# Kernel tuning notes

Hardware: AMD Instinct MI355X
Metric: run time of the kernel (lower is better)

The kernel has to match this reference:

```python
import jax, jax.numpy as jnp
import numpy as np

N_NODES = 100000
N_EDGES = 1600000
IN_F = 128
OUT_F = 128
EDGE_F = 16


def setup_inputs() -> dict:
    key = jax.random.key(0)
    ks = jax.random.split(key, 8)
    H = jax.random.normal(ks[0], (N_NODES, IN_F), dtype=jnp.float32)
    edge_index = jax.random.randint(ks[1], (2, N_EDGES), 0, N_ODES_ := N_NODES, dtype=jnp.int64) if False else jax.random.randint(ks[1], (2, N_EDGES), 0, N_NODES, dtype=jnp.int32).astype(jnp.int64)
    edge_attr = jax.random.normal(ks[2], (N_EDGES, EDGE_F), dtype=jnp.float32)
    We = jax.random.normal(ks[3], (EDGE_F, IN_F), dtype=jnp.float32) * (1.0 / np.sqrt(EDGE_F))
    be = jnp.zeros((IN_F,), dtype=jnp.float32)
    W1 = jax.random.normal(ks[4], (IN_F, OUT_F), dtype=jnp.float32) * (1.0 / np.sqrt(IN_F))
    b1 = jnp.zeros((OUT_F,), dtype=jnp.float32)
    W2 = jax.random.normal(ks[5], (OUT_F, OUT_F), dtype=jnp.float32) * (1.0 / np.sqrt(OUT_F))
    b2 = jnp.zeros((OUT_F,), dtype=jnp.float32)
    return {"H": H, "edge_index": edge_index, "edge_attr": edge_attr,
            "We": We, "be": be, "W1": W1, "b1": b1, "W2": W2, "b2": b2}


def reference(H, edge_index, edge_attr, We, be, W1, b1, W2, b2):
    # edge_mlp: Linear(edge_attr_dim -> in_features)
    edge_messages = edge_attr @ We + be                       # [E, in_f]
    # gather by src, add edge messages
    messages = H[edge_index[0]] + edge_messages               # [E, in_f]
    # scatter_add by dst with dim_size = N
    aggregated = jax.ops.segment_sum(messages, edge_index[1], num_segments=H.shape[0])  # [N, in_f]
    # node_mlp: Linear -> ReLU -> Linear
    h = jax.nn.relu(aggregated @ W1 + b1)                     # [N, out_f]
    out = h @ W2 + b2                                         # [N, out_f]
    return out
```

## Files before the change

### kernel.cpp

```cpp
#include <hip/hip_runtime.h>

#define IN_F 128
#define EF 16

typedef short bf16x8 __attribute__((ext_vector_type(8)));
typedef float f32x4  __attribute__((ext_vector_type(4)));

__device__ __forceinline__ unsigned short f2b(float f) {
    unsigned b = __float_as_uint(f);
    b += 0x7fffu + ((b >> 16) & 1u);
    return (unsigned short)(b >> 16);
}
__device__ __forceinline__ float blo(unsigned u) { return __uint_as_float(u << 16); }
__device__ __forceinline__ float bhi(unsigned u) { return __uint_as_float(u & 0xffff0000u); }


__global__ __launch_bounds__(256) void hist_kernel(
    const int* __restrict__ ei, int* __restrict__ counts, int E)
{
    int e = blockIdx.x * 256 + threadIdx.x;
    if (e >= E) return;
    atomicAdd(&counts[ei[E + e]], 1);
}

__global__ __launch_bounds__(256) void scan_blocks_kernel(
    const int* __restrict__ in, int* __restrict__ out,
    int* __restrict__ partials, int n)
{
    __shared__ int sdata[256];
    const int t = threadIdx.x;
    const int idx0 = blockIdx.x * 1024 + t * 4;
    int v[4];
    #pragma unroll
    for (int i = 0; i < 4; i++) { int idx = idx0 + i; v[i] = (idx < n) ? in[idx] : 0; }
    int s = v[0] + v[1] + v[2] + v[3];
    sdata[t] = s;
    __syncthreads();
    for (int off = 1; off < 256; off <<= 1) {
        int x = (t >= off) ? sdata[t - off] : 0;
        __syncthreads();
        sdata[t] += x;
        __syncthreads();
    }
    if (t == 255) partials[blockIdx.x] = sdata[255];
    int run = (t > 0) ? sdata[t - 1] : 0;
    #pragma unroll
    for (int i = 0; i < 4; i++) {
        int idx = idx0 + i;
        if (idx < n) out[idx] = run;
        run += v[i];
    }
}

__global__ void scan_partials_kernel(int* partials, int B)
{
    __shared__ int sdata[1024];
    const int t = threadIdx.x;
    sdata[t] = (t < B) ? partials[t] : 0;
    __syncthreads();
    for (int off = 1; off < 1024; off <<= 1) {
        int x = (t >= off) ? sdata[t - off] : 0;
        __syncthreads();
        sdata[t] += x;
        __syncthreads();
    }
    if (t < B) partials[t] = (t > 0) ? sdata[t - 1] : 0;
}

__global__ __launch_bounds__(256) void scan_add_kernel(
    int* __restrict__ out, const int* __restrict__ partials, int n)
{
    int idx = blockIdx.x * 256 + threadIdx.x;
    if (idx < n) out[idx] += partials[idx >> 10];
}

__global__ __launch_bounds__(256) void build_kernel(
    const int* __restrict__ ei, int2* __restrict__ sorted,
    const int* __restrict__ offsets, int* __restrict__ cursor, int E)
{
    int e = blockIdx.x * 256 + threadIdx.x;
    if (e >= E) return;
    int src = ei[e];
    int dst = ei[E + e];
    int pos = offsets[dst] + atomicAdd(&cursor[dst], 1);
    sorted[pos] = make_int2(src, e);
}

__global__ __launch_bounds__(256) void h2b_kernel(
    const float* __restrict__ H, unsigned short* __restrict__ Hb, int n4)
{
    int i = blockIdx.x * 256 + threadIdx.x;
    if (i >= n4) return;
    float4 v = ((const float4*)H)[i];
    ushort4 r;
    r.x = f2b(v.x); r.y = f2b(v.y); r.z = f2b(v.z); r.w = f2b(v.w);
    ((ushort4*)Hb)[i] = r;
}

__global__ __launch_bounds__(256) void gather_bf16_kernel(
    const unsigned short* __restrict__ Hb,
    const float* __restrict__ EA,
    const int2* __restrict__ sorted,
    const int* __restrict__ offsets,
    float* __restrict__ agg,
    float* __restrict__ aggE,
    float* __restrict__ degf,
    int N)
{
    int n = blockIdx.x * 4 + (threadIdx.x >> 6);
    if (n >= N) return;
    int lane = threadIdx.x & 63;
    int half = lane >> 5;
    int l32  = lane & 31;
    int s = offsets[n];
    int e_end = offsets[n + 1];
    float a0 = 0.f, a1 = 0.f, a2 = 0.f, a3 = 0.f, accE = 0.f;
    int i = s + half;
    for (; i + 6 < e_end; i += 8) {
        int2 s0 = sorted[i];
        int2 s1 = sorted[i + 2];
        int2 s2 = sorted[i + 4];
        int2 s3 = sorted[i + 6];
        uint2 u0 = *(const uint2*)(Hb + (long long)s0.x * IN_F + l32 * 4);
        uint2 u1 = *(const uint2*)(Hb + (long long)s1.x * IN_F + l32 * 4);
        uint2 u2 = *(const uint2*)(Hb + (long long)s2.x * IN_F + l32 * 4);
        uint2 u3 = *(const uint2*)(Hb + (long long)s3.x * IN_F + l32 * 4);
        float e0 = 0.f, e1 = 0.f, e2 = 0.f, e3 = 0.f;
        if (l32 < EF) {
            e0 = EA[(long long)s0.y * EF + l32];
            e1 = EA[(long long)s1.y * EF + l32];
            e2 = EA[(long long)s2.y * EF + l32];
            e3 = EA[(long long)s3.y * EF + l32];
        }
        a0 += (blo(u0.x) + blo(u1.x)) + (blo(u2.x) + blo(u3.x));
        a1 += (bhi(u0.x) + bhi(u1.x)) + (bhi(u2.x) + bhi(u3.x));
        a2 += (blo(u0.y) + blo(u1.y)) + (blo(u2.y) + blo(u3.y));
        a3 += (bhi(u0.y) + bhi(u1.y)) + (bhi(u2.y) + bhi(u3.y));
        accE += (e0 + e1) + (e2 + e3);
    }
    for (; i < e_end; i += 2) {
        int2 se = sorted[i];
        uint2 u = *(const uint2*)(Hb + (long long)se.x * IN_F + l32 * 4);
        a0 += blo(u.x); a1 += bhi(u.x); a2 += blo(u.y); a3 += bhi(u.y);
        if (l32 < EF) accE += EA[(long long)se.y * EF + l32];
    }
    a0 += __shfl_xor(a0, 32, 64);
    a1 += __shfl_xor(a1, 32, 64);
    a2 += __shfl_xor(a2, 32, 64);
    a3 += __shfl_xor(a3, 32, 64);
    accE += __shfl_xor(accE, 32, 64);
    if (half == 0) {
        *(float4*)(agg + (long long)n * IN_F + l32 * 4) = make_float4(a0, a1, a2, a3);
        if (l32 < EF) aggE[n * EF + l32] = accE;
        if (l32 == 0) degf[n] = (float)(e_end - s);
    }
}

__global__ __launch_bounds__(256) void gather_f32_kernel(
    const float* __restrict__ H,
    const float* __restrict__ EA,
    const int2* __restrict__ sorted,
    const int* __restrict__ offsets,
    float* __restrict__ agg,
    float* __restrict__ aggE,
    float* __restrict__ degf,
    int N)
{
    int n = blockIdx.x * 4 + (threadIdx.x >> 6);
    if (n >= N) return;
    int lane = threadIdx.x & 63;
    int half = lane >> 5;
    int l32  = lane & 31;
    int s = offsets[n];
    int e_end = offsets[n + 1];
    float4 acc = make_float4(0.f, 0.f, 0.f, 0.f);
    float accE = 0.f;
    int i = s + half;
    for (; i + 6 < e_end; i += 8) {
        int2 s0 = sorted[i];
        int2 s1 = sorted[i + 2];
        int2 s2 = sorted[i + 4];
        int2 s3 = sorted[i + 6];
        float4 v0 = *(const float4*)(H + (long long)s0.x * IN_F + l32 * 4);
        float4 v1 = *(const float4*)(H + (long long)s1.x * IN_F + l32 * 4);
        float4 v2 = *(const float4*)(H + (long long)s2.x * IN_F + l32 * 4);
        float4 v3 = *(const float4*)(H + (long long)s3.x * IN_F + l32 * 4);
        float e0 = 0.f, e1 = 0.f, e2 = 0.f, e3 = 0.f;
        if (l32 < EF) {
            e0 = EA[(long long)s0.y * EF + l32];
            e1 = EA[(long long)s1.y * EF + l32];
            e2 = EA[(long long)s2.y * EF + l32];
            e3 = EA[(long long)s3.y * EF + l32];
        }
        acc.x += (v0.x + v1.x) + (v2.x + v3.x);
        acc.y += (v0.y + v1.y) + (v2.y + v3.y);
        acc.z += (v0.z + v1.z) + (v2.z + v3.z);
        acc.w += (v0.w + v1.w) + (v2.w + v3.w);
        accE  += (e0 + e1) + (e2 + e3);
    }
    for (; i < e_end; i += 2) {
        int2 se = sorted[i];
        float4 v = *(const float4*)(H + (long long)se.x * IN_F + l32 * 4);
        acc.x += v.x; acc.y += v.y; acc.z += v.z; acc.w += v.w;
        if (l32 < EF) accE += EA[(long long)se.y * EF + l32];
    }
    acc.x += __shfl_xor(acc.x, 32, 64);
    acc.y += __shfl_xor(acc.y, 32, 64);
    acc.z += __shfl_xor(acc.z, 32, 64);
    acc.w += __shfl_xor(acc.w, 32, 64);
    accE  += __shfl_xor(accE, 32, 64);
    if (half == 0) {
        *(float4*)(agg + (long long)n * IN_F + l32 * 4) = acc;
        if (l32 < EF) aggE[n * EF + l32] = accE;
        if (l32 == 0) degf[n] = (float)(e_end - s);
    }
}

__global__ __launch_bounds__(256) void edge_scatter_kernel(
    const float* __restrict__ H,
    const int* __restrict__ ei,
    const float* __restrict__ EA,
    float* __restrict__ agg,
    float* __restrict__ aggE,
    float* __restrict__ deg,
    int E)
{
    long long gid = (long long)blockIdx.x * 256 + threadIdx.x;
    int e = (int)(gid >> 7);
    if (e >= E) return;
    int f = (int)(gid & 127);
    int src = ei[e];
    int dst = ei[E + e];
    float m = H[(long long)src * IN_F + f];
    atomicAdd(&agg[(long long)dst * IN_F + f], m);
    if (f < EF) atomicAdd(&aggE[dst * EF + f], EA[e * EF + f]);
    if (f == 0) atomicAdd(&deg[dst], 1.0f);
}


__global__ __launch_bounds__(256) void prep_kernel(
    const float* __restrict__ agg, const float* __restrict__ aggE,
    const float* __restrict__ degf,
    const float* __restrict__ We, const float* __restrict__ be,
    unsigned short* __restrict__ Ab, int N)
{
    int r = blockIdx.x * 8 + (threadIdx.x >> 5);
    if (r >= N) return;
    int c4 = (threadIdx.x & 31) * 4;
    float4 v = *(const float4*)&agg[(long long)r * IN_F + c4];
    float d = degf[r];
    float4 bev = *(const float4*)&be[c4];
    v.x += d * bev.x; v.y += d * bev.y; v.z += d * bev.z; v.w += d * bev.w;
    #pragma unroll
    for (int k = 0; k < EF; k++) {
        float a = aggE[r * EF + k];
        float4 w = *(const float4*)&We[k * IN_F + c4];
        v.x += a * w.x; v.y += a * w.y; v.z += a * w.z; v.w += a * w.w;
    }
    ushort4 o;
    o.x = f2b(v.x); o.y = f2b(v.y); o.z = f2b(v.z); o.w = f2b(v.w);
    *(ushort4*)&Ab[(long long)r * IN_F + c4] = o;
}

__global__ __launch_bounds__(256) void wt_cast_kernel(
    const float* __restrict__ W, unsigned short* __restrict__ Wt)
{
    int idx = blockIdx.x * 256 + threadIdx.x;
    int n = idx >> 7, k = idx & 127;
    Wt[n * IN_F + k] = f2b(W[k * IN_F + n]);
}

#define XPITCH 136
__global__ __launch_bounds__(256) void mlp_mfma_kernel(
    const unsigned short* __restrict__ Ab,
    const unsigned short* __restrict__ W1t,
    const unsigned short* __restrict__ W2t,
    const float* __restrict__ b1, const float* __restrict__ b2,
    float* __restrict__ out, int N)
{
    __shared__ unsigned short sW[128 * XPITCH];
    __shared__ unsigned short sX[64 * XPITCH];
    const int t    = threadIdx.x;
    const int tile = blockIdx.x * 64;
    const int lane = t & 63;
    const int wv   = t >> 6;
    const int quad = lane >> 4;
    const int lr   = lane & 15;
    const int M0   = wv * 16;

    {
        const uint4 z = make_uint4(0, 0, 0, 0);
        #pragma unroll
        for (int j = 0; j < 4; j++) {
            int idx = t + 256 * j;
            int row = idx >> 4, c = idx & 15;
            uint4 v = z;
            if (tile + row < N) v = ((const uint4*)Ab)[(long long)(tile + row) * 16 + c];
            ((uint4*)sX)[row * 17 + c] = v;
        }
        #pragma unroll
        for (int j = 0; j < 8; j++) {
            int idx = t + 256 * j;
            int row = idx >> 4, c = idx & 15;
            ((uint4*)sW)[row * 17 + c] = ((const uint4*)W1t)[idx];
        }
    }
    __syncthreads();

    f32x4 acc[8];
    bf16x8 af[4];
    const f32x4 zero = {0.f, 0.f, 0.f, 0.f};

    #pragma unroll
    for (int kt = 0; kt < 4; kt++)
        af[kt] = *(const bf16x8*)&sX[(M0 + lr) * XPITCH + kt * 32 + quad * 8];
    #pragma unroll
    for (int nt = 0; nt < 8; nt++) {
        acc[nt] = zero;
        #pragma unroll
        for (int kt = 0; kt < 4; kt++) {
            bf16x8 bf = *(const bf16x8*)&sW[(nt * 16 + lr) * XPITCH + kt * 32 + quad * 8];
            acc[nt] = __builtin_amdgcn_mfma_f32_16x16x32_bf16(af[kt], bf, acc[nt], 0, 0, 0);
        }
    }
    #pragma unroll
    for (int nt = 0; nt < 8; nt++) {
        int col = nt * 16 + lr;
        float bias = b1[col];
        #pragma unroll
        for (int r = 0; r < 4; r++) {
            float v = fmaxf(acc[nt][r] + bias, 0.f);
            sX[(M0 + quad * 4 + r) * XPITCH + col] = f2b(v);
        }
    }
    __syncthreads();
    #pragma unroll
    for (int j = 0; j < 8; j++) {
        int idx = t + 256 * j;
        int row = idx >> 4, c = idx & 15;
        ((uint4*)sW)[row * 17 + c] = ((const uint4*)W2t)[idx];
    }
    __syncthreads();

    #pragma unroll
    for (int kt = 0; kt < 4; kt++)
        af[kt] = *(const bf16x8*)&sX[(M0 + lr) * XPITCH + kt * 32 + quad * 8];
    #pragma unroll
    for (int nt = 0; nt < 8; nt++) {
        acc[nt] = zero;
        #pragma unroll
        for (int kt = 0; kt < 4; kt++) {
            bf16x8 bf = *(const bf16x8*)&sW[(nt * 16 + lr) * XPITCH + kt * 32 + quad * 8];
            acc[nt] = __builtin_amdgcn_mfma_f32_16x16x32_bf16(af[kt], bf, acc[nt], 0, 0, 0);
        }
    }
    #pragma unroll
    for (int nt = 0; nt < 8; nt++) {
        int col = nt * 16 + lr;
        float bias = b2[col];
        #pragma unroll
        for (int r = 0; r < 4; r++) {
            int row = tile + M0 + quad * 4 + r;
            if (row < N) out[(long long)row * IN_F + col] = acc[nt][r] + bias;
        }
    }
}

__global__ __launch_bounds__(256) void node_mlp_kernel(
    float* agg_out,
    const float* __restrict__ aggE,
    const float* __restrict__ degf,
    const float* __restrict__ We, const float* __restrict__ be,
    const float* __restrict__ W1, const float* __restrict__ b1,
    const float* __restrict__ W2, const float* __restrict__ b2,
    int N)
{
    __shared__ float sA[32][IN_F];
    __shared__ float sH[32][IN_F];
    const int t  = threadIdx.x;
    const int c4 = (t & 31) * 4;
    const int r0 = t >> 5;

    const int tile = blockIdx.x * 32;
    if (tile >= N) return;
    int rows = N - tile;
    if (rows > 32) rows = 32;

    {
        const float4 bev = *(const float4*)&be[c4];
        #pragma unroll
        for (int i = 0; i < 4; i++) {
            int rr = r0 + 8 * i;
            float4 v = make_float4(0.f, 0.f, 0.f, 0.f);
            if (rr < rows) {
                long long r = tile + rr;
                v = *(const float4*)&agg_out[r * IN_F + c4];
                float d = degf[r];
                v.x += d * bev.x; v.y += d * bev.y; v.z += d * bev.z; v.w += d * bev.w;
                #pragma unroll
                for (int k = 0; k < EF; k++) {
                    float a = aggE[r * EF + k];
                    float4 w = *(const float4*)&We[k * IN_F + c4];
                    v.x += a * w.x; v.y += a * w.y; v.z += a * w.z; v.w += a * w.w;
                }
            }
            *(float4*)&sA[rr][c4] = v;
        }
    }
    __syncthreads();
    {
        const float4 bv = *(const float4*)&b1[c4];
        float4 a0 = bv, a1 = bv, a2 = bv, a3 = bv;
        for (int k = 0; k < IN_F; k++) {
            float4 w = *(const float4*)&W1[k * IN_F + c4];
            float x0 = sA[r0][k], x1 = sA[r0 + 8][k], x2 = sA[r0 + 16][k], x3 = sA[r0 + 24][k];
            a0.x += x0 * w.x; a0.y += x0 * w.y; a0.z += x0 * w.z; a0.w += x0 * w.w;
            a1.x += x1 * w.x; a1.y += x1 * w.y; a1.z += x1 * w.z; a1.w += x1 * w.w;
            a2.x += x2 * w.x; a2.y += x2 * w.y; a2.z += x2 * w.z; a2.w += x2 * w.w;
            a3.x += x3 * w.x; a3.y += x3 * w.y; a3.z += x3 * w.z; a3.w += x3 * w.w;
        }
        a0.x = fmaxf(a0.x, 0.f); a0.y = fmaxf(a0.y, 0.f); a0.z = fmaxf(a0.z, 0.f); a0.w = fmaxf(a0.w, 0.f);
        a1.x = fmaxf(a1.x, 0.f); a1.y = fmaxf(a1.y, 0.f); a1.z = fmaxf(a1.z, 0.f); a1.w = fmaxf(a1.w, 0.f);
        a2.x = fmaxf(a2.x, 0.f); a2.y = fmaxf(a2.y, 0.f); a2.z = fmaxf(a2.z, 0.f); a2.w = fmaxf(a2.w, 0.f);
        a3.x = fmaxf(a3.x, 0.f); a3.y = fmaxf(a3.y, 0.f); a3.z = fmaxf(a3.z, 0.f); a3.w = fmaxf(a3.w, 0.f);
        *(float4*)&sH[r0][c4]      = a0;
        *(float4*)&sH[r0 + 8][c4]  = a1;
        *(float4*)&sH[r0 + 16][c4] = a2;
        *(float4*)&sH[r0 + 24][c4] = a3;
    }
    __syncthreads();
    {
        const float4 bv = *(const float4*)&b2[c4];
        float4 a0 = bv, a1 = bv, a2 = bv, a3 = bv;
        for (int k = 0; k < IN_F; k++) {
            float4 w = *(const float4*)&W2[k * IN_F + c4];
            float x0 = sH[r0][k], x1 = sH[r0 + 8][k], x2 = sH[r0 + 16][k], x3 = sH[r0 + 24][k];
            a0.x += x0 * w.x; a0.y += x0 * w.y; a0.z += x0 * w.z; a0.w += x0 * w.w;
            a1.x += x1 * w.x; a1.y += x1 * w.y; a1.z += x1 * w.z; a1.w += x1 * w.w;
            a2.x += x2 * w.x; a2.y += x2 * w.y; a2.z += x2 * w.z; a2.w += x2 * w.w;
            a3.x += x3 * w.x; a3.y += x3 * w.y; a3.z += x3 * w.z; a3.w += x3 * w.w;
        }
        #pragma unroll
        for (int i = 0; i < 4; i++) {
            int rr = r0 + 8 * i;
            if (rr < rows) {
                float4 v = (i == 0) ? a0 : (i == 1) ? a1 : (i == 2) ? a2 : a3;
                *(float4*)&agg_out[(long long)(tile + rr) * IN_F + c4] = v;
            }
        }
    }
}

extern "C" void kernel_launch(void* const* d_in, const int* in_sizes, int n_in,
                              void* d_out, int out_size, void* d_ws, size_t ws_size,
                              hipStream_t stream) {
    const float* H  = (const float*)d_in[0];
    const int*   ei = (const int*)d_in[1];
    const float* EA = (const float*)d_in[2];
    const float* We = (const float*)d_in[3];
    const float* be = (const float*)d_in[4];
    const float* W1 = (const float*)d_in[5];
    const float* b1 = (const float*)d_in[6];
    const float* W2 = (const float*)d_in[7];
    const float* b2 = (const float*)d_in[8];
    float* out = (float*)d_out;

    const int N = in_sizes[0] / IN_F;
    const int E = in_sizes[2] / EF;

    char* p = (char*)d_ws;
    auto alloc = [&](size_t bytes) { char* r = p; p += (bytes + 255) & ~(size_t)255; return r; };
    int2*  sorted   = (int2*)alloc((size_t)E * sizeof(int2));
    float* aggE     = (float*)alloc((size_t)N * EF * sizeof(float));
    float* degf     = (float*)alloc((size_t)N * sizeof(float));
    int*   counts   = (int*)alloc((size_t)(N + 1) * sizeof(int));
    int*   offsets  = (int*)alloc((size_t)(N + 1) * sizeof(int));
    int*   cursor   = (int*)alloc((size_t)N * sizeof(int));
    int*   partials = (int*)alloc(1024 * sizeof(int));
    size_t need_base = (size_t)(p - (char*)d_ws);
    unsigned short* Hb = (unsigned short*)alloc((size_t)N * IN_F * sizeof(unsigned short));
    size_t need_bf16 = (size_t)(p - (char*)d_ws);
    unsigned short* Ab  = (unsigned short*)alloc((size_t)N * IN_F * sizeof(unsigned short));
    unsigned short* W1t = (unsigned short*)alloc((size_t)IN_F * IN_F * sizeof(unsigned short));
    unsigned short* W2t = (unsigned short*)alloc((size_t)IN_F * IN_F * sizeof(unsigned short));
    size_t need_mfma = (size_t)(p - (char*)d_ws);

    const int n_scan = N + 1;
    const int B = (n_scan + 1023) / 1024;

    bool mfma_path = false;
    if (ws_size >= need_base && B <= 1024) {
        hipMemsetAsync(counts, 0, (size_t)(N + 1) * sizeof(int), stream);
        hipMemsetAsync(cursor, 0, (size_t)N * sizeof(int), stream);
        hist_kernel<<<(E + 255) / 256, 256, 0, stream>>>(ei, counts, E);
        scan_blocks_kernel<<<B, 256, 0, stream>>>(counts, offsets, partials, n_scan);
        scan_partials_kernel<<<1, 1024, 0, stream>>>(partials, B);
        scan_add_kernel<<<(n_scan + 255) / 256, 256, 0, stream>>>(offsets, partials, n_scan);
        build_kernel<<<(E + 255) / 256, 256, 0, stream>>>(ei, sorted, offsets, cursor, E);
        if (ws_size >= need_bf16) {
            int n4 = N * IN_F / 4;
            h2b_kernel<<<(n4 + 255) / 256, 256, 0, stream>>>(H, Hb, n4);
            gather_bf16_kernel<<<(N + 3) / 4, 256, 0, stream>>>(Hb, EA, sorted, offsets, out, aggE, degf, N);
        } else {
            gather_f32_kernel<<<(N + 3) / 4, 256, 0, stream>>>(H, EA, sorted, offsets, out, aggE, degf, N);
        }
        mfma_path = (ws_size >= need_mfma);
    } else {
        float* f_aggE = (float*)d_ws;
        float* f_deg  = f_aggE + (size_t)N * EF;
        aggE = f_aggE; degf = f_deg;
        hipMemsetAsync(d_out, 0, (size_t)N * IN_F * sizeof(float), stream);
        hipMemsetAsync(d_ws, 0, (size_t)N * (EF + 1) * sizeof(float), stream);
        long long tot = (long long)E * IN_F;
        edge_scatter_kernel<<<(int)((tot + 255) / 256), 256, 0, stream>>>(H, ei, EA, out, f_aggE, f_deg, E);
    }

    if (mfma_path) {
        wt_cast_kernel<<<64, 256, 0, stream>>>(W1, W1t);
        wt_cast_kernel<<<64, 256, 0, stream>>>(W2, W2t);
        prep_kernel<<<(N + 7) / 8, 256, 0, stream>>>(out, aggE, degf, We, be, Ab, N);
        mlp_mfma_kernel<<<(N + 63) / 64, 256, 0, stream>>>(Ab, W1t, W2t, b1, b2, out, N);
    } else {
        node_mlp_kernel<<<(N + 31) / 32, 256, 0, stream>>>(out, aggE, degf, We, be, W1, b1, W2, b2, N);
    }
}
```

Measured before the change: 548.5 us.

## Fuse preprocessing kernels, merge scan passes, fold edge projection into gather

Merges H-to-bf16 conversion, the destination histogram and both weight transposes into one multi-role launch. The partial-sum scan is folded into the add pass: each block sums the preceding partials itself. The edge-MLP projection and bias are applied inside the gather kernel, which writes bf16 Ab directly, removing the fp32 agg/aggE/deg round trip and the separate prep kernel. Counts and cursor are zeroed with a single memset. This cuts launch count and global memory traffic, at the cost of more per-wave work in the gather (16 shuffles plus We loads) and some redundant partial summation in the scan.

```diff
diff --git a/kernel.cpp b/kernel.cpp
--- a/kernel.cpp
+++ b/kernel.cpp
@@ -14,6 +14,35 @@
 __device__ __forceinline__ float blo(unsigned u) { return __uint_as_float(u << 16); }
 __device__ __forceinline__ float bhi(unsigned u) { return __uint_as_float(u & 0xffff0000u); }
 
+
+__global__ __launch_bounds__(256) void pre_kernel(
+    const float* __restrict__ H, unsigned short* __restrict__ Hb, int n4,
+    const int* __restrict__ ei, int* __restrict__ counts, int E,
+    const float* __restrict__ W1, unsigned short* __restrict__ W1t,
+    const float* __restrict__ W2, unsigned short* __restrict__ W2t,
+    int h2b_blocks, int hist_blocks)
+{
+    int b = blockIdx.x;
+    if (b < h2b_blocks) {
+        int i = b * 256 + threadIdx.x;
+        if (i < n4) {
+            float4 v = ((const float4*)H)[i];
+            ushort4 r;
+            r.x = f2b(v.x); r.y = f2b(v.y); r.z = f2b(v.z); r.w = f2b(v.w);
+            ((ushort4*)Hb)[i] = r;
+        }
+    } else if (b < h2b_blocks + hist_blocks) {
+        int e = (b - h2b_blocks) * 256 + threadIdx.x;
+        if (e < E) atomicAdd(&counts[ei[E + e]], 1);
+    } else {
+        int idx = (b - h2b_blocks - hist_blocks) * 256 + threadIdx.x;
+        int w = idx >> 14;
+        int r = idx & 16383;
+        int n = r >> 7, k = r & 127;
+        if (w == 0) W1t[n * IN_F + k] = f2b(W1[k * IN_F + n]);
+        else        W2t[n * IN_F + k] = f2b(W2[k * IN_F + n]);
+    }
+}
 
 __global__ __launch_bounds__(256) void hist_kernel(
     const int* __restrict__ ei, int* __restrict__ counts, int E)
@@ -52,26 +81,21 @@
     }
 }
 
-__global__ void scan_partials_kernel(int* partials, int B)
-{
-    __shared__ int sdata[1024];
+__global__ __launch_bounds__(256) void scan_add_fused_kernel(
+    int* __restrict__ out, const int* __restrict__ partials, int n)
+{
+    __shared__ int sw[4];
     const int t = threadIdx.x;
-    sdata[t] = (t < B) ? partials[t] : 0;
-    __syncthreads();
-    for (int off = 1; off < 1024; off <<= 1) {
-        int x = (t >= off) ? sdata[t - off] : 0;
-        __syncthreads();
-        sdata[t] += x;
-        __syncthreads();
-    }
-    if (t < B) partials[t] = (t > 0) ? sdata[t - 1] : 0;
-}
-
-__global__ __launch_bounds__(256) void scan_add_kernel(
-    int* __restrict__ out, const int* __restrict__ partials, int n)
-{
-    int idx = blockIdx.x * 256 + threadIdx.x;
-    if (idx < n) out[idx] += partials[idx >> 10];
+    const int g = blockIdx.x >> 2;
+    int v = 0;
+    for (int j = t; j < g; j += 256) v += partials[j];
+    #pragma unroll
+    for (int off = 1; off < 64; off <<= 1) v += __shfl_xor(v, off, 64);
+    if ((t & 63) == 0) sw[t >> 6] = v;
+    __syncthreads();
+    int P = sw[0] + sw[1] + sw[2] + sw[3];
+    int idx = blockIdx.x * 256 + t;
+    if (idx < n) out[idx] += P;
 }
 
 __global__ __launch_bounds__(256) void build_kernel(
@@ -86,25 +110,14 @@
     sorted[pos] = make_int2(src, e);
 }
 
-__global__ __launch_bounds__(256) void h2b_kernel(
-    const float* __restrict__ H, unsigned short* __restrict__ Hb, int n4)
-{
-    int i = blockIdx.x * 256 + threadIdx.x;
-    if (i >= n4) return;
-    float4 v = ((const float4*)H)[i];
-    ushort4 r;
-    r.x = f2b(v.x); r.y = f2b(v.y); r.z = f2b(v.z); r.w = f2b(v.w);
-    ((ushort4*)Hb)[i] = r;
-}
-
-__global__ __launch_bounds__(256) void gather_bf16_kernel(
+__global__ __launch_bounds__(256) void gather_fused_kernel(
     const unsigned short* __restrict__ Hb,
     const float* __restrict__ EA,
     const int2* __restrict__ sorted,
     const int* __restrict__ offsets,
-    float* __restrict__ agg,
-    float* __restrict__ aggE,
-    float* __restrict__ degf,
+    const float* __restrict__ We,
+    const float* __restrict__ be,
+    unsigned short* __restrict__ Ab,
     int N)
 {
     int n = blockIdx.x * 4 + (threadIdx.x >> 6);
@@ -149,10 +162,24 @@
     a2 += __shfl_xor(a2, 32, 64);
     a3 += __shfl_xor(a3, 32, 64);
     accE += __shfl_xor(accE, 32, 64);
+
+    const int c4 = l32 * 4;
+    const float deg = (float)(e_end - s);
+    float4 bev = *(const float4*)&be[c4];
+    float vx = a0 + deg * bev.x;
+    float vy = a1 + deg * bev.y;
+    float vz = a2 + deg * bev.z;
+    float vw = a3 + deg * bev.w;
+    #pragma unroll
+    for (int k = 0; k < EF; k++) {
+        float ak = __shfl(accE, k, 64);
+        float4 w = *(const float4*)&We[k * IN_F + c4];
+        vx += ak * w.x; vy += ak * w.y; vz += ak * w.z; vw += ak * w.w;
+    }
     if (half == 0) {
-        *(float4*)(agg + (long long)n * IN_F + l32 * 4) = make_float4(a0, a1, a2, a3);
-        if (l32 < EF) aggE[n * EF + l32] = accE;
-        if (l32 == 0) degf[n] = (float)(e_end - s);
+        ushort4 o;
+        o.x = f2b(vx); o.y = f2b(vy); o.z = f2b(vz); o.w = f2b(vw);
+        *(ushort4*)&Ab[(long long)n * IN_F + c4] = o;
     }
 }
 
@@ -238,38 +265,6 @@
 }
 
 
-__global__ __launch_bounds__(256) void prep_kernel(
-    const float* __restrict__ agg, const float* __restrict__ aggE,
-    const float* __restrict__ degf,
-    const float* __restrict__ We, const float* __restrict__ be,
-    unsigned short* __restrict__ Ab, int N)
-{
-    int r = blockIdx.x * 8 + (threadIdx.x >> 5);
-    if (r >= N) return;
-    int c4 = (threadIdx.x & 31) * 4;
-    float4 v = *(const float4*)&agg[(long long)r * IN_F + c4];
-    float d = degf[r];
-    float4 bev = *(const float4*)&be[c4];
-    v.x += d * bev.x; v.y += d * bev.y; v.z += d * bev.z; v.w += d * bev.w;
-    #pragma unroll
-    for (int k = 0; k < EF; k++) {
-        float a = aggE[r * EF + k];
-        float4 w = *(const float4*)&We[k * IN_F + c4];
-        v.x += a * w.x; v.y += a * w.y; v.z += a * w.z; v.w += a * w.w;
-    }
-    ushort4 o;
-    o.x = f2b(v.x); o.y = f2b(v.y); o.z = f2b(v.z); o.w = f2b(v.w);
-    *(ushort4*)&Ab[(long long)r * IN_F + c4] = o;
-}
-
-__global__ __launch_bounds__(256) void wt_cast_kernel(
-    const float* __restrict__ W, unsigned short* __restrict__ Wt)
-{
-    int idx = blockIdx.x * 256 + threadIdx.x;
-    int n = idx >> 7, k = idx & 127;
-    Wt[n * IN_F + k] = f2b(W[k * IN_F + n]);
-}
-
 #define XPITCH 136
 __global__ __launch_bounds__(256) void mlp_mfma_kernel(
     const unsigned short* __restrict__ Ab,
@@ -474,12 +469,11 @@
     float* aggE     = (float*)alloc((size_t)N * EF * sizeof(float));
     float* degf     = (float*)alloc((size_t)N * sizeof(float));
     int*   counts   = (int*)alloc((size_t)(N + 1) * sizeof(int));
+    int*   cursor   = (int*)alloc((size_t)N * sizeof(int));
     int*   offsets  = (int*)alloc((size_t)(N + 1) * sizeof(int));
-    int*   cursor   = (int*)alloc((size_t)N * sizeof(int));
     int*   partials = (int*)alloc(1024 * sizeof(int));
     size_t need_base = (size_t)(p - (char*)d_ws);
     unsigned short* Hb = (unsigned short*)alloc((size_t)N * IN_F * sizeof(unsigned short));
-    size_t need_bf16 = (size_t)(p - (char*)d_ws);
     unsigned short* Ab  = (unsigned short*)alloc((size_t)N * IN_F * sizeof(unsigned short));
     unsigned short* W1t = (unsigned short*)alloc((size_t)IN_F * IN_F * sizeof(unsigned short));
     unsigned short* W2t = (unsigned short*)alloc((size_t)IN_F * IN_F * sizeof(unsigned short));
@@ -487,40 +481,35 @@
 
     const int n_scan = N + 1;
     const int B = (n_scan + 1023) / 1024;
-
-    bool mfma_path = false;
-    if (ws_size >= need_base && B <= 1024) {
-        hipMemsetAsync(counts, 0, (size_t)(N + 1) * sizeof(int), stream);
-        hipMemsetAsync(cursor, 0, (size_t)N * sizeof(int), stream);
+    const size_t zero_bytes = (size_t)((char*)offsets - (char*)counts);
+
+    if (ws_size >= need_mfma && B <= 1024) {
+        hipMemsetAsync(counts, 0, zero_bytes, stream);
+        const int n4 = N * IN_F / 4;
+        const int h2b_blocks  = (n4 + 255) / 256;
+        const int hist_blocks = (E + 255) / 256;
+        pre_kernel<<<h2b_blocks + hist_blocks + 128, 256, 0, stream>>>(
+            H, Hb, n4, ei, counts, E, W1, W1t, W2, W2t, h2b_blocks, hist_blocks);
+        scan_blocks_kernel<<<B, 256, 0, stream>>>(counts, offsets, partials, n_scan);
+        scan_add_fused_kernel<<<(n_scan + 255) / 256, 256, 0, stream>>>(offsets, partials, n_scan);
+        build_kernel<<<(E + 255) / 256, 256, 0, stream>>>(ei, sorted, offsets, cursor, E);
+        gather_fused_kernel<<<(N + 3) / 4, 256, 0, stream>>>(Hb, EA, sorted, offsets, We, be, Ab, N);
+        mlp_mfma_kernel<<<(N + 63) / 64, 256, 0, stream>>>(Ab, W1t, W2t, b1, b2, out, N);
+    } else if (ws_size >= need_base && B <= 1024) {
+        hipMemsetAsync(counts, 0, zero_bytes, stream);
         hist_kernel<<<(E + 255) / 256, 256, 0, stream>>>(ei, counts, E);
         scan_blocks_kernel<<<B, 256, 0, stream>>>(counts, offsets, partials, n_scan);
-        scan_partials_kernel<<<1, 1024, 0, stream>>>(partials, B);
-        scan_add_kernel<<<(n_scan + 255) / 256, 256, 0, stream>>>(offsets, partials, n_scan);
+        scan_add_fused_kernel<<<(n_scan + 255) / 256, 256, 0, stream>>>(offsets, partials, n_scan);
         build_kernel<<<(E + 255) / 256, 256, 0, stream>>>(ei, sorted, offsets, cursor, E);
-        if (ws_size >= need_bf16) {
-            int n4 = N * IN_F / 4;
-            h2b_kernel<<<(n4 + 255) / 256, 256, 0, stream>>>(H, Hb, n4);
-            gather_bf16_kernel<<<(N + 3) / 4, 256, 0, stream>>>(Hb, EA, sorted, offsets, out, aggE, degf, N);
-        } else {
-            gather_f32_kernel<<<(N + 3) / 4, 256, 0, stream>>>(H, EA, sorted, offsets, out, aggE, degf, N);
-        }
-        mfma_path = (ws_size >= need_mfma);
+        gather_f32_kernel<<<(N + 3) / 4, 256, 0, stream>>>(H, EA, sorted, offsets, out, aggE, degf, N);
+        node_mlp_kernel<<<(N + 31) / 32, 256, 0, stream>>>(out, aggE, degf, We, be, W1, b1, W2, b2, N);
     } else {
         float* f_aggE = (float*)d_ws;
         float* f_deg  = f_aggE + (size_t)N * EF;
-        aggE = f_aggE; degf = f_deg;
         hipMemsetAsync(d_out, 0, (size_t)N * IN_F * sizeof(float), stream);
         hipMemsetAsync(d_ws, 0, (size_t)N * (EF + 1) * sizeof(float), stream);
         long long tot = (long long)E * IN_F;
         edge_scatter_kernel<<<(int)((tot + 255) / 256), 256, 0, stream>>>(H, ei, EA, out, f_aggE, f_deg, E);
-    }
-
-    if (mfma_path) {
-        wt_cast_kernel<<<64, 256, 0, stream>>>(W1, W1t);
-        wt_cast_kernel<<<64, 256, 0, stream>>>(W2, W2t);
-        prep_kernel<<<(N + 7) / 8, 256, 0, stream>>>(out, aggE, degf, We, be, Ab, N);
-        mlp_mfma_kernel<<<(N + 63) / 64, 256, 0, stream>>>(Ab, W1t, W2t, b1, b2, out, N);
-    } else {
-        node_mlp_kernel<<<(N + 31) / 32, 256, 0, stream>>>(out, aggE, degf, We, be, W1, b1, W2, b2, N);
-    }
-}
+        node_mlp_kernel<<<(N + 31) / 32, 256, 0, stream>>>(out, f_aggE, f_deg, We, be, W1, b1, W2, b2, N);
+    }
+}
```

After: 505.2 us. 7.9% less time.
